# Performance work log

Hardware: AMD Instinct MI355X
Metric: run time of the kernel (lower is better)

## Reference

```python
import jax, jax.numpy as jnp
import numpy as np

B, S, E, H = 2, 4096, 512, 8
DK = E // H


def setup_inputs() -> dict:
    k = jax.random.key(0)
    ks = jax.random.split(k, 11)
    sc = 0.02
    return {
        "query": jax.random.normal(ks[0], (B, S, E), jnp.float32),
        "key_in": jax.random.normal(ks[1], (B, S, E), jnp.float32),
        "value": jax.random.normal(ks[2], (B, S, E), jnp.float32),
        "Wq": jax.random.normal(ks[3], (E, E), jnp.float32) * sc,
        "bq": jax.random.normal(ks[4], (E,), jnp.float32) * sc,
        "Wk": jax.random.normal(ks[5], (E, E), jnp.float32) * sc,
        "bk": jax.random.normal(ks[6], (E,), jnp.float32) * sc,
        "Wv": jax.random.normal(ks[7], (E, E), jnp.float32) * sc,
        "bv": jax.random.normal(ks[8], (E,), jnp.float32) * sc,
        "Wo": jax.random.normal(ks[9], (E, E), jnp.float32) * sc,
        "bo": jax.random.normal(ks[10], (E,), jnp.float32) * sc,
    }


def reference(query, key_in, value, Wq, bq, Wk, bk, Wv, bv, Wo, bo):
    b, s, _ = query.shape
    # Linear projections
    q = query @ Wq + bq
    k = key_in @ Wk + bk
    v = value @ Wv + bv
    # [b, s, H, dk] -> [b, H, s, dk]
    q = q.reshape(b, s, H, DK).transpose(0, 2, 1, 3)
    k = k.reshape(b, s, H, DK).transpose(0, 2, 1, 3)
    v = v.reshape(b, s, H, DK).transpose(0, 2, 1, 3)
    # NOTE: source bug — softmax over UNSCALED scores (1/sqrt scaling in the
    # original is applied to a dead variable after softmax). Reproduce faithfully.
    scores = jnp.einsum("bhqd,bhkd->bhqk", q, k)  # [b,H,s,s] — O(N^2) materialized
    weights = jax.nn.softmax(scores.astype(jnp.float32), axis=-1)
    attn = jnp.einsum("bhqk,bhkd->bhqd", weights, v)
    # [b,H,s,dk] -> [b,s,E]
    concat = attn.transpose(0, 2, 1, 3).reshape(b, s, E)
    return concat @ Wo + bo
```

## Files before the change

### kernel.cpp

```cpp
#include <hip/hip_runtime.h>
#include <hip/hip_bf16.h>

#define B_  2
#define S_  4096
#define E_  512
#define H_  8
#define DK_ 64
#define M_  8192

typedef float f32x4  __attribute__((ext_vector_type(4)));
typedef float f32x16 __attribute__((ext_vector_type(16)));
typedef short s16x8  __attribute__((ext_vector_type(8)));
typedef short s16x4  __attribute__((ext_vector_type(4)));

static __device__ __forceinline__ short f2bf(float x) {
  __hip_bfloat16 h = __float2bfloat16(x);
  return __builtin_bit_cast(short, h);
}

static __device__ __forceinline__ f32x4 mfma32(s16x8 a, s16x8 b, f32x4 c) {
  return __builtin_amdgcn_mfma_f32_16x16x32_bf16(a, b, c, 0, 0, 0);
}

static __device__ __forceinline__ f32x16 mfma3232(s16x8 a, s16x8 b, f32x16 c) {
  return __builtin_amdgcn_mfma_f32_32x32x16_bf16(a, b, c, 0, 0, 0);
}

static __device__ __forceinline__ float fastexp2(float x) {
#if __has_builtin(__builtin_amdgcn_exp2f)
  return __builtin_amdgcn_exp2f(x);
#else
  return __expf(x * 0.69314718056f);
#endif
}

static __device__ __forceinline__ void gload_lds16(const void* g, void* l) {
  __builtin_amdgcn_global_load_lds(
      (const __attribute__((address_space(1))) unsigned int*)g,
      (__attribute__((address_space(3))) unsigned int*)l, 16, 0, 0);
}

__global__ __launch_bounds__(256) void conv_bf16_all(
    const float* __restrict__ q, const float* __restrict__ k,
    const float* __restrict__ v, short* __restrict__ out, int n4) {
  const float* in = (blockIdx.y == 0) ? q : ((blockIdx.y == 1) ? k : v);
  short* o = out + (size_t)blockIdx.y * (size_t)n4 * 4;
  int i = blockIdx.x * 256 + threadIdx.x;
  if (i < n4) {
    float4 x = *((const float4*)in + i);
    s16x4 r;
    r[0] = f2bf(x.x); r[1] = f2bf(x.y); r[2] = f2bf(x.z); r[3] = f2bf(x.w);
    *((s16x4*)o + i) = r;
  }
}

__global__ __launch_bounds__(256) void conv_wT_all(
    const float* __restrict__ Wq, const float* __restrict__ Wk,
    const float* __restrict__ Wv, const float* __restrict__ Wo,
    short* __restrict__ Wt) {
  const float* W = (blockIdx.y == 0) ? Wq
                   : ((blockIdx.y == 1) ? Wk : ((blockIdx.y == 2) ? Wv : Wo));
  short* o = Wt + (size_t)blockIdx.y * (E_ * E_);
  int idx = blockIdx.x * 256 + threadIdx.x;
  int j = idx >> 9, k = idx & 511;
  o[idx] = f2bf(W[(size_t)k * E_ + j]);
}

static __device__ __forceinline__ void gemm_core_512(
    const short* __restrict__ A, const short* __restrict__ Bt,
    short* As, short* Bs, int tm, int tn, f32x4 acc[4][4]) {
  const int tid = threadIdx.x;
  const int wave = tid >> 6, lane = tid & 63;
  const int wm = (wave >> 1) * 64, wn = (wave & 1) * 64;
  const int c = lane & 15, g = lane >> 4;
  for (int kk = 0; kk < 512; kk += 64) {
#pragma unroll
    for (int i = 0; i < 4; ++i) {
      int ob = wave * 4096 + i * 1024 + lane * 16;
      int row = ob >> 7;
      int col = (ob & 127) >> 1;
      gload_lds16(A + (size_t)(tm + row) * 512 + kk + col,
                  (char*)As + wave * 4096 + i * 1024);
      gload_lds16(Bt + (size_t)(tn + row) * 512 + kk + col,
                  (char*)Bs + wave * 4096 + i * 1024);
    }
    __syncthreads();
#pragma unroll
    for (int s = 0; s < 2; ++s) {
      s16x8 af[4], bfr[4];
#pragma unroll
      for (int i = 0; i < 4; ++i)
        af[i] = *(const s16x8*)&As[(wm + i * 16 + c) * 64 + s * 32 + g * 8];
#pragma unroll
      for (int j = 0; j < 4; ++j)
        bfr[j] = *(const s16x8*)&Bs[(wn + j * 16 + c) * 64 + s * 32 + g * 8];
#pragma unroll
      for (int i = 0; i < 4; ++i)
#pragma unroll
        for (int j = 0; j < 4; ++j)
          acc[i][j] = mfma32(af[i], bfr[j], acc[i][j]);
    }
    __syncthreads();
  }
}

__global__ __launch_bounds__(256) void gemm_qkv(
    const short* __restrict__ Xq, const short* __restrict__ Xk,
    const short* __restrict__ Xv, const short* __restrict__ Wt,
    const float* __restrict__ bq, const float* __restrict__ bk,
    const float* __restrict__ bv,
    short* __restrict__ Qo, short* __restrict__ Ko, short* __restrict__ Vto) {
  __shared__ __align__(16) short As[128 * 64];
  __shared__ __align__(16) short Bs[128 * 64];
  const int z = blockIdx.z;
  const short* A = (z == 0) ? Xq : ((z == 1) ? Xk : Xv);
  const short* Bt = Wt + z * (E_ * E_);
  const float* bias = (z == 0) ? bq : ((z == 1) ? bk : bv);
  const int tm = blockIdx.x * 128, tn = blockIdx.y * 128;
  f32x4 acc[4][4] = {};
  gemm_core_512(A, Bt, As, Bs, tm, tn, acc);

  const int tid = threadIdx.x;
  const int wave = tid >> 6, lane = tid & 63;
  const int wm = (wave >> 1) * 64, wn = (wave & 1) * 64;
  const int c = lane & 15, g = lane >> 4;
#pragma unroll
  for (int i = 0; i < 4; ++i) {
#pragma unroll
    for (int j = 0; j < 4; ++j) {
      const int gc = tn + wn + j * 16 + c;
      const float bb = bias[gc];
      const int h = gc >> 6, dk = gc & 63;
#pragma unroll
      for (int r = 0; r < 4; ++r) {
        const int gr = tm + wm + i * 16 + g * 4 + r;
        const int b = gr >> 12, s = gr & 4095;
        float v = acc[i][j][r] + bb;
        if (z == 0) v *= 1.44269504f;
        const short hv = f2bf(v);
        if (z == 2)
          Vto[(size_t)((b * H_ + h) * DK_ + dk) * S_ + s] = hv;
        else if (z == 1)
          Ko[(size_t)((b * H_ + h) * S_ + s) * DK_ + dk] = hv;
        else
          Qo[(size_t)((b * H_ + h) * S_ + s) * DK_ + dk] = hv;
      }
    }
  }
}

__global__ __launch_bounds__(256) void gemm_out(
    const short* __restrict__ AO, const short* __restrict__ Wot,
    const float* __restrict__ bo, float* __restrict__ out) {
  __shared__ __align__(16) short As[128 * 64];
  __shared__ __align__(16) short Bs[128 * 64];
  const int tm = blockIdx.x * 128, tn = blockIdx.y * 128;
  f32x4 acc[4][4] = {};
  gemm_core_512(AO, Wot, As, Bs, tm, tn, acc);

  const int tid = threadIdx.x;
  const int wave = tid >> 6, lane = tid & 63;
  const int wm = (wave >> 1) * 64, wn = (wave & 1) * 64;
  const int c = lane & 15, g = lane >> 4;
#pragma unroll
  for (int i = 0; i < 4; ++i) {
#pragma unroll
    for (int j = 0; j < 4; ++j) {
      const int gc = tn + wn + j * 16 + c;
      const float bb = bo[gc];
#pragma unroll
      for (int r = 0; r < 4; ++r) {
        const int gr = tm + wm + i * 16 + g * 4 + r;
        out[(size_t)gr * E_ + gc] = acc[i][j][r] + bb;
      }
    }
  }
}

__global__ __launch_bounds__(512, 2) void attn_fwd(
    const short* __restrict__ Q, const short* __restrict__ K,
    const short* __restrict__ Vt, short* __restrict__ O) {
  __shared__ __align__(16) short Ks[2][64 * 64];
  __shared__ __align__(16) short Vs[3][64 * 64];
  const int tid = threadIdx.x;
  const int wave = tid >> 6, lane = tid & 63;
  const int role = wave >> 2;
  const int qi = lane & 31, hi = lane >> 5;
  const int bh = blockIdx.y;
  const int b = bh >> 3, h = bh & 7;
  const int q0 = blockIdx.x * 256 + wave * 32;
  const short* Qp = Q + (size_t)bh * S_ * DK_;
  const short* Kp = K + (size_t)bh * S_ * DK_;
  const short* Vp = Vt + (size_t)bh * DK_ * S_;

  s16x8 qf[4];
#pragma unroll
  for (int s = 0; s < 4; ++s)
    qf[s] = *(const s16x8*)(Qp + (size_t)(q0 + qi) * DK_ + s * 16 + hi * 8);

  f32x16 o0 = {}, o1 = {};
  f32x16 lacc = {};
  s16x8 ones;
#pragma unroll
  for (int e = 0; e < 8; ++e) ones[e] = (short)0x3F80;

  int kOff, vOff;
  {
    const int j = wave;
    const int row = (j >> 2) * 32 + qi;
    const int srow = (row & 32) | ((row & 8) << 1) | ((row & 4) << 1) |
                     ((row & 16) >> 2) | (row & 3);
    kOff = srow * DK_ + (j & 3) * 16 + hi * 8;
    vOff = ((j >> 2) * 32 + qi) * S_ + ((j >> 1) & 1) * 32 +
           (j & 1) * 16 + hi * 8;
  }

  auto stage = [&](int kt) {
    gload_lds16(Kp + (size_t)kt * 64 * DK_ + kOff,
                (char*)Ks[kt & 1] + wave * 1024);
    gload_lds16(Vp + (size_t)kt * 64 + vOff,
                (char*)Vs[kt % 3] + wave * 1024);
  };

  const int lb = lane << 4;

  auto qk = [&](const short* Kbuf, f32x16& s0, f32x16& s1) {
    const char* Kc = (const char*)Kbuf + lb;
    f32x16 t0 = {}, t1 = {};
    __builtin_amdgcn_s_setprio(1);
#pragma unroll
    for (int s = 0; s < 4; ++s) {
      s16x8 ka = *(const s16x8*)(Kc + s * 1024);
      s16x8 kb = *(const s16x8*)(Kc + 4096 + s * 1024);
      t0 = mfma3232(ka, qf[s], t0);
      t1 = mfma3232(kb, qf[s], t1);
    }
    __builtin_amdgcn_s_setprio(0);
    s0 = t0; s1 = t1;
  };

  auto softpv = [&](const f32x16& s0, const f32x16& s1, const short* Vbuf) {
    const char* Vc = (const char*)Vbuf + lb;
    float p0[16], p1[16];
#pragma unroll
    for (int r = 0; r < 16; ++r) { p0[r] = fastexp2(s0[r]); p1[r] = fastexp2(s1[r]); }
    s16x8 pb[2][2];
#pragma unroll
    for (int ks = 0; ks < 2; ++ks)
#pragma unroll
      for (int j = 0; j < 8; ++j) {
        const int r = (j & 3) | (ks << 2) | ((j >> 2) << 3);
        pb[0][ks][j] = f2bf(p0[r]);
        pb[1][ks][j] = f2bf(p1[r]);
      }
    __builtin_amdgcn_s_setprio(1);
#pragma unroll
    for (int hf = 0; hf < 2; ++hf)
#pragma unroll
      for (int ks = 0; ks < 2; ++ks) {
        s16x8 va0 = *(const s16x8*)(Vc + (hf * 2 + ks) * 1024);
        s16x8 va1 = *(const s16x8*)(Vc + 4096 + (hf * 2 + ks) * 1024);
        o0 = mfma3232(va0, pb[hf][ks], o0);
        o1 = mfma3232(va1, pb[hf][ks], o1);
        lacc = mfma3232(ones, pb[hf][ks], lacc);
      }
    __builtin_amdgcn_s_setprio(0);
  };

  const int NT = S_ / 64;
  f32x16 sp0, sp1;

  stage(0);
  __syncthreads();

  for (int t = 0; t < NT; ++t) {
    if (t + 1 < NT) stage(t + 1);
    if (role == 0) {
      qk(Ks[t & 1], sp0, sp1);
      softpv(sp0, sp1, Vs[t % 3]);
    } else {
      if (t > 0) softpv(sp0, sp1, Vs[(t - 1) % 3]);
      qk(Ks[t & 1], sp0, sp1);
    }
    __syncthreads();
  }
  if (role == 1) softpv(sp0, sp1, Vs[(NT - 1) % 3]);

  const float rl = 1.f / lacc[0];
  short* Op = O + ((size_t)(b * S_ + q0 + qi)) * E_ + h * DK_;
#pragma unroll
  for (int rr = 0; rr < 4; ++rr) {
    s16x4 ov0, ov1;
#pragma unroll
    for (int e = 0; e < 4; ++e) {
      ov0[e] = f2bf(o0[rr * 4 + e] * rl);
      ov1[e] = f2bf(o1[rr * 4 + e] * rl);
    }
    *(s16x4*)(Op + rr * 8 + hi * 4) = ov0;
    *(s16x4*)(Op + 32 + rr * 8 + hi * 4) = ov1;
  }
}

extern "C" void kernel_launch(void* const* d_in, const int* in_sizes, int n_in,
                              void* d_out, int out_size, void* d_ws, size_t ws_size,
                              hipStream_t stream) {
  const float* query  = (const float*)d_in[0];
  const float* key_in = (const float*)d_in[1];
  const float* value  = (const float*)d_in[2];
  const float* Wq = (const float*)d_in[3];
  const float* bq = (const float*)d_in[4];
  const float* Wk = (const float*)d_in[5];
  const float* bk = (const float*)d_in[6];
  const float* Wv = (const float*)d_in[7];
  const float* bv = (const float*)d_in[8];
  const float* Wo = (const float*)d_in[9];
  const float* bo = (const float*)d_in[10];
  float* out = (float*)d_out;

  const size_t NA = (size_t)M_ * E_;
  short* ws  = (short*)d_ws;
  short* Xq  = ws;
  short* Wt  = Xq + 3 * NA;
  short* Wot = Wt + 3 * E_ * E_;
  short* Qb  = Wt + 4 * E_ * E_;
  short* Kb  = Qb + NA;
  short* Vtb = Kb + NA;
  short* AO  = Vtb + NA;
  short* Xk  = Xq + NA;
  short* Xv  = Xk + NA;

  conv_bf16_all<<<dim3(NA / 1024, 3), 256, 0, stream>>>(
      query, key_in, value, Xq, (int)(NA / 4));
  conv_wT_all<<<dim3(E_ * E_ / 256, 4), 256, 0, stream>>>(Wq, Wk, Wv, Wo, Wt);

  gemm_qkv<<<dim3(M_ / 128, E_ / 128, 3), 256, 0, stream>>>(
      Xq, Xk, Xv, Wt, bq, bk, bv, Qb, Kb, Vtb);
  attn_fwd<<<dim3(S_ / 256, B_ * H_), 512, 0, stream>>>(Qb, Kb, Vtb, AO);
  gemm_out<<<dim3(M_ / 128, E_ / 128), 256, 0, stream>>>(AO, Wot, bo, out);
}
```

Baseline: 168.5 us.

## Split KV tile across wave pairs with 64-row query blocks and LDS merge

Each pair of waves now owns 64 query rows, and the two waves split each 64-key tile between them. Every K and V fragment read from LDS therefore feeds two MFMAs. The row-sum is computed with scalar adds instead of an extra ones-MFMA. The two-role software pipeline is replaced by a uniform two-tile ping-pong schedule, and partial outputs and sums are merged through LDS at the end. The aim is fewer LDS reads and fewer MFMAs per unit of work, at the cost of more registers, an LDS reduction epilogue and half the waves idling during the store.

```diff
diff --git a/kernel.cpp b/kernel.cpp
--- a/kernel.cpp
+++ b/kernel.cpp
@@ -180,29 +180,27 @@
 __global__ __launch_bounds__(512, 2) void attn_fwd(
     const short* __restrict__ Q, const short* __restrict__ K,
     const short* __restrict__ Vt, short* __restrict__ O) {
-  __shared__ __align__(16) short Ks[2][64 * 64];
-  __shared__ __align__(16) short Vs[3][64 * 64];
+  __shared__ __align__(16) char lds[40960];
   const int tid = threadIdx.x;
   const int wave = tid >> 6, lane = tid & 63;
-  const int role = wave >> 2;
+  const int g = wave >> 1, kh = wave & 1;
   const int qi = lane & 31, hi = lane >> 5;
   const int bh = blockIdx.y;
   const int b = bh >> 3, h = bh & 7;
-  const int q0 = blockIdx.x * 256 + wave * 32;
+  const int q0 = blockIdx.x * 256 + g * 64;
   const short* Qp = Q + (size_t)bh * S_ * DK_;
   const short* Kp = K + (size_t)bh * S_ * DK_;
   const short* Vp = Vt + (size_t)bh * DK_ * S_;
 
-  s16x8 qf[4];
-#pragma unroll
-  for (int s = 0; s < 4; ++s)
-    qf[s] = *(const s16x8*)(Qp + (size_t)(q0 + qi) * DK_ + s * 16 + hi * 8);
-
-  f32x16 o0 = {}, o1 = {};
-  f32x16 lacc = {};
-  s16x8 ones;
-#pragma unroll
-  for (int e = 0; e < 8; ++e) ones[e] = (short)0x3F80;
+  s16x8 qfL[4], qfH[4];
+#pragma unroll
+  for (int s = 0; s < 4; ++s) {
+    qfL[s] = *(const s16x8*)(Qp + (size_t)(q0 + qi) * DK_ + s * 16 + hi * 8);
+    qfH[s] = *(const s16x8*)(Qp + (size_t)(q0 + 32 + qi) * DK_ + s * 16 + hi * 8);
+  }
+
+  f32x16 o00 = {}, o01 = {}, o10 = {}, o11 = {};
+  float lsL = 0.f, lsH = 0.f;
 
   int kOff, vOff;
   {
@@ -217,87 +215,140 @@
 
   auto stage = [&](int kt) {
     gload_lds16(Kp + (size_t)kt * 64 * DK_ + kOff,
-                (char*)Ks[kt & 1] + wave * 1024);
+                lds + (kt & 1) * 8192 + wave * 1024);
     gload_lds16(Vp + (size_t)kt * 64 + vOff,
-                (char*)Vs[kt % 3] + wave * 1024);
+                lds + 16384 + (kt % 3) * 8192 + wave * 1024);
   };
 
-  const int lb = lane << 4;
-
-  auto qk = [&](const short* Kbuf, f32x16& s0, f32x16& s1) {
-    const char* Kc = (const char*)Kbuf + lb;
-    f32x16 t0 = {}, t1 = {};
+  const int lbK = kh * 4096 + (lane << 4);
+
+  auto qk = [&](int t, f32x16& sL, f32x16& sH) {
+    const char* Kc = lds + (t & 1) * 8192 + lbK;
+    f32x16 a = {}, c = {};
     __builtin_amdgcn_s_setprio(1);
 #pragma unroll
     for (int s = 0; s < 4; ++s) {
       s16x8 ka = *(const s16x8*)(Kc + s * 1024);
-      s16x8 kb = *(const s16x8*)(Kc + 4096 + s * 1024);
-      t0 = mfma3232(ka, qf[s], t0);
-      t1 = mfma3232(kb, qf[s], t1);
+      a = mfma3232(ka, qfL[s], a);
+      c = mfma3232(ka, qfH[s], c);
     }
     __builtin_amdgcn_s_setprio(0);
-    s0 = t0; s1 = t1;
+    sL = a; sH = c;
   };
 
-  auto softpv = [&](const f32x16& s0, const f32x16& s1, const short* Vbuf) {
-    const char* Vc = (const char*)Vbuf + lb;
-    float p0[16], p1[16];
-#pragma unroll
-    for (int r = 0; r < 16; ++r) { p0[r] = fastexp2(s0[r]); p1[r] = fastexp2(s1[r]); }
-    s16x8 pb[2][2];
+  auto softpv = [&](const f32x16& sL, const f32x16& sH, int t) {
+    const char* Vc = lds + 16384 + (t % 3) * 8192 + kh * 2048 + (lane << 4);
+    float pL[16], pH[16];
+#pragma unroll
+    for (int r = 0; r < 16; ++r) { pL[r] = fastexp2(sL[r]); pH[r] = fastexp2(sH[r]); }
+    float aL = 0.f, aH = 0.f;
+#pragma unroll
+    for (int r = 0; r < 16; ++r) { aL += pL[r]; aH += pH[r]; }
+    lsL += aL; lsH += aH;
+    s16x8 pbL[2], pbH[2];
 #pragma unroll
     for (int ks = 0; ks < 2; ++ks)
 #pragma unroll
       for (int j = 0; j < 8; ++j) {
         const int r = (j & 3) | (ks << 2) | ((j >> 2) << 3);
-        pb[0][ks][j] = f2bf(p0[r]);
-        pb[1][ks][j] = f2bf(p1[r]);
+        pbL[ks][j] = f2bf(pL[r]);
+        pbH[ks][j] = f2bf(pH[r]);
       }
     __builtin_amdgcn_s_setprio(1);
 #pragma unroll
-    for (int hf = 0; hf < 2; ++hf)
-#pragma unroll
-      for (int ks = 0; ks < 2; ++ks) {
-        s16x8 va0 = *(const s16x8*)(Vc + (hf * 2 + ks) * 1024);
-        s16x8 va1 = *(const s16x8*)(Vc + 4096 + (hf * 2 + ks) * 1024);
-        o0 = mfma3232(va0, pb[hf][ks], o0);
-        o1 = mfma3232(va1, pb[hf][ks], o1);
-        lacc = mfma3232(ones, pb[hf][ks], lacc);
-      }
+    for (int ks = 0; ks < 2; ++ks) {
+      s16x8 va0 = *(const s16x8*)(Vc + ks * 1024);
+      s16x8 va1 = *(const s16x8*)(Vc + 4096 + ks * 1024);
+      o00 = mfma3232(va0, pbL[ks], o00);
+      o01 = mfma3232(va0, pbH[ks], o01);
+      o10 = mfma3232(va1, pbL[ks], o10);
+      o11 = mfma3232(va1, pbH[ks], o11);
+    }
     __builtin_amdgcn_s_setprio(0);
   };
 
   const int NT = S_ / 64;
-  f32x16 sp0, sp1;
+  f32x16 sA0, sA1, sB0, sB1;
 
   stage(0);
   __syncthreads();
-
-  for (int t = 0; t < NT; ++t) {
-    if (t + 1 < NT) stage(t + 1);
-    if (role == 0) {
-      qk(Ks[t & 1], sp0, sp1);
-      softpv(sp0, sp1, Vs[t % 3]);
-    } else {
-      if (t > 0) softpv(sp0, sp1, Vs[(t - 1) % 3]);
-      qk(Ks[t & 1], sp0, sp1);
-    }
+  stage(1);
+  qk(0, sA0, sA1);
+  __syncthreads();
+
+  for (int t = 0; t < NT; t += 2) {
+    if (t + 2 < NT) stage(t + 2);
+    qk(t + 1, sB0, sB1);
+    softpv(sA0, sA1, t);
     __syncthreads();
-  }
-  if (role == 1) softpv(sp0, sp1, Vs[(NT - 1) % 3]);
-
-  const float rl = 1.f / lacc[0];
-  short* Op = O + ((size_t)(b * S_ + q0 + qi)) * E_ + h * DK_;
-#pragma unroll
-  for (int rr = 0; rr < 4; ++rr) {
-    s16x4 ov0, ov1;
-#pragma unroll
-    for (int e = 0; e < 4; ++e) {
-      ov0[e] = f2bf(o0[rr * 4 + e] * rl);
-      ov1[e] = f2bf(o1[rr * 4 + e] * rl);
-    }
-    *(s16x4*)(Op + rr * 8 + hi * 4) = ov0;
-    *(s16x4*)(Op + 32 + rr * 8 + hi * 4) = ov1;
+    if (t + 3 < NT) stage(t + 3);
+    if (t + 2 < NT) qk(t + 2, sA0, sA1);
+    softpv(sB0, sB1, t + 1);
+    __syncthreads();
+  }
+
+  lsL += __shfl_xor(lsL, 32);
+  lsH += __shfl_xor(lsH, 32);
+
+  float* mrg = (float*)lds;
+  const int mi = (g * 64 + lane) * 36;
+  __syncthreads();
+  if (kh) {
+#pragma unroll
+    for (int r = 0; r < 4; ++r) {
+      *(f32x4*)(mrg + mi + r * 4) =
+          f32x4{o00[r * 4], o00[r * 4 + 1], o00[r * 4 + 2], o00[r * 4 + 3]};
+      *(f32x4*)(mrg + mi + 16 + r * 4) =
+          f32x4{o01[r * 4], o01[r * 4 + 1], o01[r * 4 + 2], o01[r * 4 + 3]};
+    }
+    mrg[mi + 32] = lsL;
+    mrg[mi + 33] = lsH;
+  }
+  __syncthreads();
+  float rlL = 0.f, rlH = 0.f;
+  if (!kh) {
+#pragma unroll
+    for (int r = 0; r < 16; ++r) {
+      o00[r] += mrg[mi + r];
+      o01[r] += mrg[mi + 16 + r];
+    }
+    rlL = 1.f / (lsL + mrg[mi + 32]);
+    rlH = 1.f / (lsH + mrg[mi + 33]);
+  }
+  __syncthreads();
+  if (kh) {
+#pragma unroll
+    for (int r = 0; r < 4; ++r) {
+      *(f32x4*)(mrg + mi + r * 4) =
+          f32x4{o10[r * 4], o10[r * 4 + 1], o10[r * 4 + 2], o10[r * 4 + 3]};
+      *(f32x4*)(mrg + mi + 16 + r * 4) =
+          f32x4{o11[r * 4], o11[r * 4 + 1], o11[r * 4 + 2], o11[r * 4 + 3]};
+    }
+  }
+  __syncthreads();
+  if (!kh) {
+#pragma unroll
+    for (int r = 0; r < 16; ++r) {
+      o10[r] += mrg[mi + r];
+      o11[r] += mrg[mi + 16 + r];
+    }
+    short* OpL = O + ((size_t)(b * S_ + q0 + qi)) * E_ + h * DK_;
+    short* OpH = O + ((size_t)(b * S_ + q0 + 32 + qi)) * E_ + h * DK_;
+#pragma unroll
+    for (int rr = 0; rr < 4; ++rr) {
+      s16x4 vL0, vL1, vH0, vH1;
+#pragma unroll
+      for (int e = 0; e < 4; ++e) {
+        vL0[e] = f2bf(o00[rr * 4 + e] * rlL);
+        vL1[e] = f2bf(o10[rr * 4 + e] * rlL);
+        vH0[e] = f2bf(o01[rr * 4 + e] * rlH);
+        vH1[e] = f2bf(o11[rr * 4 + e] * rlH);
+      }
+      *(s16x4*)(OpL + rr * 8 + hi * 4) = vL0;
+      *(s16x4*)(OpL + 32 + rr * 8 + hi * 4) = vL1;
+      *(s16x4*)(OpH + rr * 8 + hi * 4) = vH0;
+      *(s16x4*)(OpH + 32 + rr * 8 + hi * 4) = vH1;
+    }
   }
 }
 
```

Measured after the change: 154.1 us. 8.6% less time.
